# Kernel tuning notes

Measured on AMD Instinct MI355X. Metric: run time of the kernel, lower is better.

The kernel has to match this reference:

```python
import jax, jax.numpy as jnp
import numpy as np

N = 100000        # nodes
E = 3200000       # edges (avg degree 32)
D_IN, D_H, D_OUT = 128, 128, 64
EPS = 1e-5        # BatchNorm eps


def setup_inputs() -> dict:
    key = jax.random.key(0)
    ks = jax.random.split(key, 12)
    s = 0.1
    return {
        "x": jax.random.normal(ks[0], (N, D_IN), jnp.float32),
        "edge_index": jax.random.randint(ks[1], (2, E), 0, N, jnp.int32),
        "W1": jax.random.normal(ks[2], (D_IN, D_H), jnp.float32) * s,
        "b1": jnp.zeros((D_H,), jnp.float32),
        "W2": jax.random.normal(ks[3], (D_H, D_H), jnp.float32) * s,
        "b2": jnp.zeros((D_H,), jnp.float32),
        "W3": jax.random.normal(ks[4], (D_H, D_OUT), jnp.float32) * s,
        "b3": jnp.zeros((D_OUT,), jnp.float32),
        "g1": jnp.ones((D_H,), jnp.float32),
        "be1": jnp.zeros((D_H,), jnp.float32),
        "g2": jnp.ones((D_H,), jnp.float32),
        "be2": jnp.zeros((D_H,), jnp.float32),
    }


def reference(x, edge_index, W1, b1, W2, b2, W3, b3, g1, be1, g2, be2):
    # GCNConv normalization: add self-loops, symmetric deg^-1/2 A deg^-1/2
    loop = jnp.arange(N, dtype=edge_index.dtype)
    src = jnp.concatenate([edge_index[0], loop])   # [E+N]
    dst = jnp.concatenate([edge_index[1], loop])   # [E+N]
    deg = jax.ops.segment_sum(jnp.ones(src.shape, x.dtype), dst, num_segments=N)
    dinv = jnp.where(deg > 0, jax.lax.rsqrt(deg), 0.0)
    norm = (dinv[src] * dinv[dst])[:, None]        # [E+N, 1]

    def conv(h, W, b):
        h = h @ W                                   # dense transform [N, d]
        msg = h[src] * norm                         # gather + scale [E+N, d]
        return jax.ops.segment_sum(msg, dst, num_segments=N) + b

    def bn(h, g, be):  # BatchNorm1d over nodes (batch stats, eval-style dropout)
        m = h.mean(axis=0)
        v = h.var(axis=0)
        return (h - m) * jax.lax.rsqrt(v + EPS) * g + be

    h = jax.nn.relu(bn(conv(x, W1, b1), g1, be1))
    h = jax.nn.relu(bn(conv(h, W2, b2), g2, be2))
    h = conv(h, W3, b3)
    return jax.nn.softmax(h, axis=1)
```

## Files before the change

### kernel.cpp

```cpp
#include <hip/hip_runtime.h>
#include <hip/hip_fp16.h>

constexpr int   NN   = 100000;
constexpr int   NE   = 3200000;
constexpr float BN_EPS = 1e-5f;

constexpr int MG_B  = (NN / 32 + 3) / 4;
constexpr int CNT_B = NE / 256;
constexpr int SC_B  = NN * 128 / 4 / 256;

typedef _Float16 half8 __attribute__((ext_vector_type(8)));
typedef float    floatx16 __attribute__((ext_vector_type(16)));

__global__ __launch_bounds__(256) void k_wprep_all(const float* __restrict__ W1,
                                                   const float* __restrict__ W2,
                                                   const float* __restrict__ W3,
                                                   _Float16* __restrict__ Wt1,
                                                   _Float16* __restrict__ Wt2,
                                                   _Float16* __restrict__ Wt3) {
  int idx = blockIdx.x * 256 + threadIdx.x;
  if (idx < 16384) {
    int k = idx >> 7, n = idx & 127;
    Wt1[n * 128 + k] = (_Float16)W1[idx];
  } else if (idx < 32768) {
    int j = idx - 16384, k = j >> 7, n = j & 127;
    Wt2[n * 128 + k] = (_Float16)W2[j];
  } else if (idx < 40960) {
    int j = idx - 32768, k = j >> 6, n = j & 63;
    Wt3[n * 128 + k] = (_Float16)W3[j];
  }
}

__global__ __launch_bounds__(256) void k_f1(const int* __restrict__ dst,
                                            int* __restrict__ deg,
                                            int* __restrict__ slot,
                                            const float* __restrict__ x,
                                            const _Float16* __restrict__ Wt1,
                                            _Float16* __restrict__ C) {
  if (blockIdx.x < MG_B) {
    int wid  = (blockIdx.x * 256 + threadIdx.x) >> 6;
    int lane = threadIdx.x & 63;
    if (wid >= NN / 32) return;
    const int m = lane & 31;
    const int q = lane >> 5;
    const int row0 = wid * 32;
    const float* Arow = x + (size_t)(row0 + m) * 128 + q * 8;

    floatx16 acc[4] = {};
#pragma unroll
    for (int s = 0; s < 8; ++s) {
      float4 a0 = *(const float4*)(Arow + 16 * s);
      float4 a1 = *(const float4*)(Arow + 16 * s + 4);
      half8 af;
      af[0] = (_Float16)a0.x; af[1] = (_Float16)a0.y;
      af[2] = (_Float16)a0.z; af[3] = (_Float16)a0.w;
      af[4] = (_Float16)a1.x; af[5] = (_Float16)a1.y;
      af[6] = (_Float16)a1.z; af[7] = (_Float16)a1.w;
#pragma unroll
      for (int ct = 0; ct < 4; ++ct) {
        half8 bf = *(const half8*)(Wt1 + (size_t)(ct * 32 + m) * 128 + q * 8 + 16 * s);
        acc[ct] = __builtin_amdgcn_mfma_f32_32x32x16_f16(af, bf, acc[ct], 0, 0, 0);
      }
    }
#pragma unroll
    for (int ct = 0; ct < 4; ++ct)
#pragma unroll
      for (int r = 0; r < 16; ++r) {
        int row = (r & 3) + 8 * (r >> 2) + 4 * q;
        C[(size_t)(row0 + row) * 128 + ct * 32 + m] = (_Float16)acc[ct][r];
      }
  } else {
    int e = (blockIdx.x - MG_B) * 256 + threadIdx.x;
    if (e < NE) slot[e] = atomicAdd(&deg[dst[e]], 1);
  }
}

__global__ __launch_bounds__(256) void k_scan_a(const int* __restrict__ deg,
                                                float* __restrict__ dinv,
                                                int* __restrict__ rowptr,
                                                int* __restrict__ bsum) {
  __shared__ int sd[256];
  int t = threadIdx.x;
  int i = blockIdx.x * 256 + t;
  int v = (i < NN) ? deg[i] : 0;
  if (i < NN) dinv[i] = rsqrtf((float)(v + 1));
  sd[t] = v;
  __syncthreads();
  for (int off = 1; off < 256; off <<= 1) {
    int x = (t >= off) ? sd[t - off] : 0;
    __syncthreads();
    sd[t] += x;
    __syncthreads();
  }
  if (i < NN) rowptr[i] = sd[t] - v;
  if (t == 255) bsum[blockIdx.x] = sd[255];
}

__global__ __launch_bounds__(512) void k_scan_b(int* __restrict__ bsum, int nb) {
  __shared__ int sd[512];
  int t = threadIdx.x;
  int v = (t < nb) ? bsum[t] : 0;
  sd[t] = v;
  __syncthreads();
  for (int off = 1; off < 512; off <<= 1) {
    int x = (t >= off) ? sd[t - off] : 0;
    __syncthreads();
    sd[t] += x;
    __syncthreads();
  }
  if (t < nb) bsum[t] = sd[t] - v;
}

__global__ __launch_bounds__(256) void k_scan_c(int* __restrict__ rowptr,
                                                const int* __restrict__ bsum) {
  int i = blockIdx.x * 256 + threadIdx.x;
  if (i < NN) rowptr[i] += bsum[blockIdx.x];
  if (i == 0) rowptr[NN] = NE;
}

__global__ __launch_bounds__(256) void k_f2(const int* __restrict__ ei,
                                            const int* __restrict__ rowptr,
                                            const int* __restrict__ slot,
                                            int* __restrict__ csrc,
                                            const float* __restrict__ dinv,
                                            uint2* __restrict__ Hf) {
  if (blockIdx.x < SC_B) {
    int i = blockIdx.x * 256 + threadIdx.x;
    int row = i >> 5;
    float dv = dinv[row];
    uint2 v = Hf[i];
    __half2 h0 = *(__half2*)&v.x;
    __half2 h1 = *(__half2*)&v.y;
    float2 f0 = __half22float2(h0);
    float2 f1 = __half22float2(h1);
    h0 = __floats2half2_rn(f0.x * dv, f0.y * dv);
    h1 = __floats2half2_rn(f1.x * dv, f1.y * dv);
    v.x = *(unsigned*)&h0;
    v.y = *(unsigned*)&h1;
    Hf[i] = v;
  } else {
    int e = (blockIdx.x - SC_B) * 256 + threadIdx.x;
    if (e >= NE) return;
    int s = ei[e];
    int d = ei[NE + e];
    csrc[rowptr[d] + slot[e]] = s;
  }
}

template <int BN_>
__global__ __launch_bounds__(256) void k_mgemm(const _Float16* __restrict__ A,
                                               const _Float16* __restrict__ Wt,
                                               const float* __restrict__ scale,
                                               const float* __restrict__ shift,
                                               const float* __restrict__ dinv,
                                               _Float16* __restrict__ C) {
  constexpr int NCT = BN_ / 32;
  int wid  = (blockIdx.x * 256 + threadIdx.x) >> 6;
  int lane = threadIdx.x & 63;
  if (wid >= NN / 32) return;
  const int m = lane & 31;
  const int q = lane >> 5;
  const int row0 = wid * 32;

  const _Float16* Arow = A + (size_t)(row0 + m) * 128 + q * 8;

  floatx16 acc[NCT] = {};

#pragma unroll
  for (int s = 0; s < 8; ++s) {
    half8 raw = *(const half8*)(Arow + 16 * s);
    int k0 = 16 * s + q * 8;
    half8 af;
#pragma unroll
    for (int j = 0; j < 8; ++j) {
      float a = fmaxf(fmaf((float)raw[j], scale[k0 + j], shift[k0 + j]), 0.f);
      af[j] = (_Float16)a;
    }
#pragma unroll
    for (int ct = 0; ct < NCT; ++ct) {
      half8 bf = *(const half8*)(Wt + (size_t)(ct * 32 + m) * 128 + q * 8 + 16 * s);
      acc[ct] = __builtin_amdgcn_mfma_f32_32x32x16_f16(af, bf, acc[ct], 0, 0, 0);
    }
  }

#pragma unroll
  for (int ct = 0; ct < NCT; ++ct)
#pragma unroll
    for (int r = 0; r < 16; ++r) {
      int row = (r & 3) + 8 * (r >> 2) + 4 * q;
      float dv = dinv[row0 + row];
      C[(size_t)(row0 + row) * BN_ + ct * 32 + m] = (_Float16)(acc[ct][r] * dv);
    }
}

__global__ __launch_bounds__(256) void k_agg128(const __half* __restrict__ H,
                                                const float* __restrict__ dinv,
                                                const int* __restrict__ rowptr,
                                                const int* __restrict__ srcs,
                                                __half2* __restrict__ out) {
  int wid  = (blockIdx.x * 256 + threadIdx.x) >> 6;
  int lane = threadIdx.x & 63;
  if (wid >= NN) return;
  const __half2* Hp = (const __half2*)H;
  float2 acc = __half22float2(Hp[(size_t)wid * 64 + lane]);
  int beg = rowptr[wid], end = rowptr[wid + 1];
  int e = beg;
  int end8 = beg + ((end - beg) & ~7);
  for (; e < end8; e += 8) {
    __half2 v0 = Hp[(size_t)srcs[e+0] * 64 + lane];
    __half2 v1 = Hp[(size_t)srcs[e+1] * 64 + lane];
    __half2 v2 = Hp[(size_t)srcs[e+2] * 64 + lane];
    __half2 v3 = Hp[(size_t)srcs[e+3] * 64 + lane];
    __half2 v4 = Hp[(size_t)srcs[e+4] * 64 + lane];
    __half2 v5 = Hp[(size_t)srcs[e+5] * 64 + lane];
    __half2 v6 = Hp[(size_t)srcs[e+6] * 64 + lane];
    __half2 v7 = Hp[(size_t)srcs[e+7] * 64 + lane];
    float2 f0 = __half22float2(v0), f1 = __half22float2(v1);
    float2 f2 = __half22float2(v2), f3 = __half22float2(v3);
    float2 f4 = __half22float2(v4), f5 = __half22float2(v5);
    float2 f6 = __half22float2(v6), f7 = __half22float2(v7);
    acc.x += (f0.x + f1.x) + (f2.x + f3.x) + (f4.x + f5.x) + (f6.x + f7.x);
    acc.y += (f0.y + f1.y) + (f2.y + f3.y) + (f4.y + f5.y) + (f6.y + f7.y);
  }
  for (; e < end; ++e) {
    float2 f = __half22float2(Hp[(size_t)srcs[e] * 64 + lane]);
    acc.x += f.x; acc.y += f.y;
  }
  float di = dinv[wid];
  out[(size_t)wid * 64 + lane] = __floats2half2_rn(acc.x * di, acc.y * di);
}

__global__ __launch_bounds__(256) void k_agg64_softmax(const __half* __restrict__ H,
                                                       const float* __restrict__ dinv,
                                                       const int* __restrict__ rowptr,
                                                       const int* __restrict__ srcs,
                                                       const float* __restrict__ b3,
                                                       float* __restrict__ out) {
  int wid  = (blockIdx.x * 256 + threadIdx.x) >> 6;
  int lane = threadIdx.x & 63;
  if (wid >= NN) return;
  float acc = __half2float(H[(size_t)wid * 64 + lane]);
  int beg = rowptr[wid], end = rowptr[wid + 1];
  int e = beg;
  int end8 = beg + ((end - beg) & ~7);
  for (; e < end8; e += 8) {
    float v0 = __half2float(H[(size_t)srcs[e+0] * 64 + lane]);
    float v1 = __half2float(H[(size_t)srcs[e+1] * 64 + lane]);
    float v2 = __half2float(H[(size_t)srcs[e+2] * 64 + lane]);
    float v3 = __half2float(H[(size_t)srcs[e+3] * 64 + lane]);
    float v4 = __half2float(H[(size_t)srcs[e+4] * 64 + lane]);
    float v5 = __half2float(H[(size_t)srcs[e+5] * 64 + lane]);
    float v6 = __half2float(H[(size_t)srcs[e+6] * 64 + lane]);
    float v7 = __half2float(H[(size_t)srcs[e+7] * 64 + lane]);
    acc += (v0 + v1) + (v2 + v3) + (v4 + v5) + (v6 + v7);
  }
  for (; e < end; ++e)
    acc += __half2float(H[(size_t)srcs[e] * 64 + lane]);
  acc = acc * dinv[wid] + b3[lane];

  float m = acc;
#pragma unroll
  for (int off = 32; off > 0; off >>= 1) m = fmaxf(m, __shfl_xor(m, off));
  float ev = __expf(acc - m);
  float s = ev;
#pragma unroll
  for (int off = 32; off > 0; off >>= 1) s += __shfl_xor(s, off);
  out[(size_t)wid * 64 + lane] = ev / s;
}

__global__ __launch_bounds__(256) void k_stats(const __half2* __restrict__ H2,
                                               float* __restrict__ S1,
                                               float* __restrict__ S2) {
  int t = threadIdx.x;
  int p = t & 63;
  int r = t >> 6;
  float2 s1 = {0.f, 0.f}, s2 = {0.f, 0.f};
  for (int row = blockIdx.x * 4 + r; row < NN; row += gridDim.x * 4) {
    float2 v = __half22float2(H2[(size_t)row * 64 + p]);
    s1.x += v.x; s1.y += v.y;
    s2.x += v.x * v.x; s2.y += v.y * v.y;
  }
  __shared__ float2 l1[256], l2[256];
  l1[t] = s1; l2[t] = s2;
  __syncthreads();
  if (t < 128) {
    l1[t].x += l1[t+128].x; l1[t].y += l1[t+128].y;
    l2[t].x += l2[t+128].x; l2[t].y += l2[t+128].y;
  }
  __syncthreads();
  if (t < 64) {
    float2 a1 = l1[t], b1 = l1[t+64];
    float2 a2 = l2[t], b2 = l2[t+64];
    atomicAdd(&S1[2*p+0], a1.x + b1.x);
    atomicAdd(&S1[2*p+1], a1.y + b1.y);
    atomicAdd(&S2[2*p+0], a2.x + b2.x);
    atomicAdd(&S2[2*p+1], a2.y + b2.y);
  }
}

__global__ void k_finalize(const float* __restrict__ S1, const float* __restrict__ S2,
                           const float* __restrict__ g,  const float* __restrict__ be,
                           float* __restrict__ scale,    float* __restrict__ shift) {
  int t = threadIdx.x;
  float mean = S1[t] * (1.0f / NN);
  float var  = S2[t] * (1.0f / NN) - mean * mean;
  float is   = rsqrtf(var + BN_EPS);
  float sc   = g[t] * is;
  scale[t] = sc;
  shift[t] = be[t] - mean * sc;
}

extern "C" void kernel_launch(void* const* d_in, const int* in_sizes, int n_in,
                              void* d_out, int out_size, void* d_ws, size_t ws_size,
                              hipStream_t stream) {
  (void)in_sizes; (void)n_in; (void)out_size; (void)ws_size;
  const float* x   = (const float*)d_in[0];
  const int*   ei  = (const int*)d_in[1];
  const float* W1  = (const float*)d_in[2];
  const float* W2  = (const float*)d_in[4];
  const float* W3  = (const float*)d_in[6];
  const float* b3  = (const float*)d_in[7];
  const float* g1  = (const float*)d_in[8];
  const float* be1 = (const float*)d_in[9];
  const float* g2  = (const float*)d_in[10];
  const float* be2 = (const float*)d_in[11];
  float* out = (float*)d_out;

  char* ws = (char*)d_ws;
  size_t off = 0;
  auto take = [&](size_t bytes) -> char* {
    char* p = ws + off;
    off = (off + bytes + 255) & ~(size_t)255;
    return p;
  };
  int*   deg    = (int*)  take((size_t)NN * 4);
  float* S1a    = (float*)take(128 * 4);
  float* S2a    = (float*)take(128 * 4);
  float* S1b    = (float*)take(128 * 4);
  float* S2b    = (float*)take(128 * 4);
  size_t zero_bytes = off;
  float* scale1 = (float*)take(128 * 4);
  float* shift1 = (float*)take(128 * 4);
  float* scale2 = (float*)take(128 * 4);
  float* shift2 = (float*)take(128 * 4);
  float* dinv   = (float*)take((size_t)NN * 4);
  int*   rowptr = (int*)  take((size_t)(NN + 1) * 4);
  int*   bsum   = (int*)  take(1024 * 4);
  int*   slot   = (int*)  take((size_t)NE * 4);
  int*   csrc   = (int*)  take((size_t)NE * 4);
  _Float16* Wt1 = (_Float16*)take((size_t)128 * 128 * 2);
  _Float16* Wt2 = (_Float16*)take((size_t)128 * 128 * 2);
  _Float16* Wt3 = (_Float16*)take((size_t)64 * 128 * 2);
  _Float16* Hf  = (_Float16*)take((size_t)NN * 128 * 2);
  _Float16* hB  = (_Float16*)take((size_t)NN * 128 * 2);

  (void)hipMemsetAsync(d_ws, 0, zero_bytes, stream);

  const int nbN  = (NN + 255) / 256;
  const int mgB  = MG_B;
  const int aggB = (NN + 3) / 4;

  k_wprep_all<<<160, 256, 0, stream>>>(W1, W2, W3, Wt1, Wt2, Wt3);

  k_f1<<<MG_B + CNT_B, 256, 0, stream>>>(ei + NE, deg, slot, x, Wt1, Hf);

  k_scan_a<<<nbN, 256, 0, stream>>>(deg, dinv, rowptr, bsum);
  k_scan_b<<<1, 512, 0, stream>>>(bsum, nbN);
  k_scan_c<<<nbN, 256, 0, stream>>>(rowptr, bsum);

  k_f2<<<SC_B + CNT_B, 256, 0, stream>>>(ei, rowptr, slot, csrc, dinv, (uint2*)Hf);

  k_agg128<<<aggB, 256, 0, stream>>>((const __half*)Hf, dinv, rowptr, csrc, (__half2*)hB);
  k_stats<<<1024, 256, 0, stream>>>((const __half2*)hB, S1a, S2a);
  k_finalize<<<1, 128, 0, stream>>>(S1a, S2a, g1, be1, scale1, shift1);

  k_mgemm<128><<<mgB, 256, 0, stream>>>(hB, Wt2, scale1, shift1, dinv, Hf);
  k_agg128<<<aggB, 256, 0, stream>>>((const __half*)Hf, dinv, rowptr, csrc, (__half2*)hB);
  k_stats<<<1024, 256, 0, stream>>>((const __half2*)hB, S1b, S2b);
  k_finalize<<<1, 128, 0, stream>>>(S1b, S2b, g2, be2, scale2, shift2);

  k_mgemm<64><<<mgB, 256, 0, stream>>>(hB, Wt3, scale2, shift2, dinv, Hf);
  k_agg64_softmax<<<aggB, 256, 0, stream>>>((const __half*)Hf, dinv, rowptr, csrc, b3, out);
}
```

Baseline: 837.8 us.

## Pack two nodes per wavefront in aggregation and merge scan into one kernel

The aggregation kernels now handle two destination nodes per 64-lane wavefront. Each half-wave gathers wider vectors (4 halves per lane for the 128-wide case, 2 per lane for the 64-wide softmax case), with predicated loads so both halves loop to the larger degree. This raises bytes per load instruction and the number of in-flight gathers per wave, at the cost of idle lanes when the two nodes' degrees differ. Separately, the three-kernel prefix scan is replaced by a single 1024-thread block that scans serial chunks, removing two launches but running the scan on one CU.

```diff
diff --git a/kernel.cpp b/kernel.cpp
--- a/kernel.cpp
+++ b/kernel.cpp
@@ -75,47 +75,31 @@
   }
 }
 
-__global__ __launch_bounds__(256) void k_scan_a(const int* __restrict__ deg,
-                                                float* __restrict__ dinv,
-                                                int* __restrict__ rowptr,
-                                                int* __restrict__ bsum) {
-  __shared__ int sd[256];
+__global__ __launch_bounds__(1024) void k_scan(const int* __restrict__ deg,
+                                               float* __restrict__ dinv,
+                                               int* __restrict__ rowptr) {
+  __shared__ int sd[1024];
   int t = threadIdx.x;
-  int i = blockIdx.x * 256 + t;
-  int v = (i < NN) ? deg[i] : 0;
-  if (i < NN) dinv[i] = rsqrtf((float)(v + 1));
-  sd[t] = v;
+  constexpr int CH = (NN + 1023) / 1024;
+  int b = t * CH, e = min(b + CH, NN);
+  int sum = 0;
+  for (int i = b; i < e; ++i) sum += deg[i];
+  sd[t] = sum;
   __syncthreads();
-  for (int off = 1; off < 256; off <<= 1) {
+  for (int off = 1; off < 1024; off <<= 1) {
     int x = (t >= off) ? sd[t - off] : 0;
     __syncthreads();
     sd[t] += x;
     __syncthreads();
   }
-  if (i < NN) rowptr[i] = sd[t] - v;
-  if (t == 255) bsum[blockIdx.x] = sd[255];
-}
-
-__global__ __launch_bounds__(512) void k_scan_b(int* __restrict__ bsum, int nb) {
-  __shared__ int sd[512];
-  int t = threadIdx.x;
-  int v = (t < nb) ? bsum[t] : 0;
-  sd[t] = v;
-  __syncthreads();
-  for (int off = 1; off < 512; off <<= 1) {
-    int x = (t >= off) ? sd[t - off] : 0;
-    __syncthreads();
-    sd[t] += x;
-    __syncthreads();
-  }
-  if (t < nb) bsum[t] = sd[t] - v;
-}
-
-__global__ __launch_bounds__(256) void k_scan_c(int* __restrict__ rowptr,
-                                                const int* __restrict__ bsum) {
-  int i = blockIdx.x * 256 + threadIdx.x;
-  if (i < NN) rowptr[i] += bsum[blockIdx.x];
-  if (i == 0) rowptr[NN] = NE;
+  int run = sd[t] - sum;
+  for (int i = b; i < e; ++i) {
+    int d = deg[i];
+    rowptr[i] = run;
+    run += d;
+    dinv[i] = rsqrtf((float)(d + 1));
+  }
+  if (t == 1023) rowptr[NN] = NE;
 }
 
 __global__ __launch_bounds__(256) void k_f2(const int* __restrict__ ei,
@@ -193,79 +177,96 @@
     }
 }
 
-__global__ __launch_bounds__(256) void k_agg128(const __half* __restrict__ H,
-                                                const float* __restrict__ dinv,
-                                                const int* __restrict__ rowptr,
-                                                const int* __restrict__ srcs,
-                                                __half2* __restrict__ out) {
-  int wid  = (blockIdx.x * 256 + threadIdx.x) >> 6;
+__global__ __launch_bounds__(256) void k_agg128p(const __half* __restrict__ H,
+                                                 const float* __restrict__ dinv,
+                                                 const int* __restrict__ rowptr,
+                                                 const int* __restrict__ srcs,
+                                                 uint2* __restrict__ out) {
+  int pw   = (blockIdx.x * 256 + threadIdx.x) >> 6;
   int lane = threadIdx.x & 63;
-  if (wid >= NN) return;
+  if (pw >= NN / 2) return;
+  const int half = lane >> 5;
+  const int node = pw * 2 + half;
+  const int c4   = lane & 31;
+  const uint2* Hp = (const uint2*)H;
+
+  uint2 sv = Hp[(size_t)node * 32 + c4];
+  __half2 s0 = *(__half2*)&sv.x, s1 = *(__half2*)&sv.y;
+  float2 a01 = __half22float2(s0);
+  float2 a23 = __half22float2(s1);
+
+  int beg = rowptr[node];
+  int cnt = rowptr[node + 1] - beg;
+  int cmax = max(__shfl(cnt, 0), __shfl(cnt, 32));
+
+  for (int i = 0; i < cmax; i += 4) {
+#pragma unroll
+    for (int j = 0; j < 4; ++j) {
+      bool p = (i + j) < cnt;
+      int pos = min(beg + (p ? i + j : 0), NE - 1);
+      int s = srcs[pos];
+      uint2 v = Hp[(size_t)s * 32 + c4];
+      __half2 h0 = *(__half2*)&v.x, h1 = *(__half2*)&v.y;
+      float2 f01 = __half22float2(h0);
+      float2 f23 = __half22float2(h1);
+      if (p) {
+        a01.x += f01.x; a01.y += f01.y;
+        a23.x += f23.x; a23.y += f23.y;
+      }
+    }
+  }
+  float di = dinv[node];
+  __half2 o0 = __floats2half2_rn(a01.x * di, a01.y * di);
+  __half2 o1 = __floats2half2_rn(a23.x * di, a23.y * di);
+  uint2 ov;
+  ov.x = *(unsigned*)&o0;
+  ov.y = *(unsigned*)&o1;
+  out[(size_t)node * 32 + c4] = ov;
+}
+
+__global__ __launch_bounds__(256) void k_agg64p_softmax(const __half* __restrict__ H,
+                                                        const float* __restrict__ dinv,
+                                                        const int* __restrict__ rowptr,
+                                                        const int* __restrict__ srcs,
+                                                        const float* __restrict__ b3,
+                                                        float* __restrict__ out) {
+  int pw   = (blockIdx.x * 256 + threadIdx.x) >> 6;
+  int lane = threadIdx.x & 63;
+  if (pw >= NN / 2) return;
+  const int half = lane >> 5;
+  const int node = pw * 2 + half;
+  const int c2   = lane & 31;
   const __half2* Hp = (const __half2*)H;
-  float2 acc = __half22float2(Hp[(size_t)wid * 64 + lane]);
-  int beg = rowptr[wid], end = rowptr[wid + 1];
-  int e = beg;
-  int end8 = beg + ((end - beg) & ~7);
-  for (; e < end8; e += 8) {
-    __half2 v0 = Hp[(size_t)srcs[e+0] * 64 + lane];
-    __half2 v1 = Hp[(size_t)srcs[e+1] * 64 + lane];
-    __half2 v2 = Hp[(size_t)srcs[e+2] * 64 + lane];
-    __half2 v3 = Hp[(size_t)srcs[e+3] * 64 + lane];
-    __half2 v4 = Hp[(size_t)srcs[e+4] * 64 + lane];
-    __half2 v5 = Hp[(size_t)srcs[e+5] * 64 + lane];
-    __half2 v6 = Hp[(size_t)srcs[e+6] * 64 + lane];
-    __half2 v7 = Hp[(size_t)srcs[e+7] * 64 + lane];
-    float2 f0 = __half22float2(v0), f1 = __half22float2(v1);
-    float2 f2 = __half22float2(v2), f3 = __half22float2(v3);
-    float2 f4 = __half22float2(v4), f5 = __half22float2(v5);
-    float2 f6 = __half22float2(v6), f7 = __half22float2(v7);
-    acc.x += (f0.x + f1.x) + (f2.x + f3.x) + (f4.x + f5.x) + (f6.x + f7.x);
-    acc.y += (f0.y + f1.y) + (f2.y + f3.y) + (f4.y + f5.y) + (f6.y + f7.y);
-  }
-  for (; e < end; ++e) {
-    float2 f = __half22float2(Hp[(size_t)srcs[e] * 64 + lane]);
-    acc.x += f.x; acc.y += f.y;
-  }
-  float di = dinv[wid];
-  out[(size_t)wid * 64 + lane] = __floats2half2_rn(acc.x * di, acc.y * di);
-}
-
-__global__ __launch_bounds__(256) void k_agg64_softmax(const __half* __restrict__ H,
-                                                       const float* __restrict__ dinv,
-                                                       const int* __restrict__ rowptr,
-                                                       const int* __restrict__ srcs,
-                                                       const float* __restrict__ b3,
-                                                       float* __restrict__ out) {
-  int wid  = (blockIdx.x * 256 + threadIdx.x) >> 6;
-  int lane = threadIdx.x & 63;
-  if (wid >= NN) return;
-  float acc = __half2float(H[(size_t)wid * 64 + lane]);
-  int beg = rowptr[wid], end = rowptr[wid + 1];
-  int e = beg;
-  int end8 = beg + ((end - beg) & ~7);
-  for (; e < end8; e += 8) {
-    float v0 = __half2float(H[(size_t)srcs[e+0] * 64 + lane]);
-    float v1 = __half2float(H[(size_t)srcs[e+1] * 64 + lane]);
-    float v2 = __half2float(H[(size_t)srcs[e+2] * 64 + lane]);
-    float v3 = __half2float(H[(size_t)srcs[e+3] * 64 + lane]);
-    float v4 = __half2float(H[(size_t)srcs[e+4] * 64 + lane]);
-    float v5 = __half2float(H[(size_t)srcs[e+5] * 64 + lane]);
-    float v6 = __half2float(H[(size_t)srcs[e+6] * 64 + lane]);
-    float v7 = __half2float(H[(size_t)srcs[e+7] * 64 + lane]);
-    acc += (v0 + v1) + (v2 + v3) + (v4 + v5) + (v6 + v7);
-  }
-  for (; e < end; ++e)
-    acc += __half2float(H[(size_t)srcs[e] * 64 + lane]);
-  acc = acc * dinv[wid] + b3[lane];
-
-  float m = acc;
-#pragma unroll
-  for (int off = 32; off > 0; off >>= 1) m = fmaxf(m, __shfl_xor(m, off));
-  float ev = __expf(acc - m);
-  float s = ev;
-#pragma unroll
-  for (int off = 32; off > 0; off >>= 1) s += __shfl_xor(s, off);
-  out[(size_t)wid * 64 + lane] = ev / s;
+
+  float2 acc = __half22float2(Hp[(size_t)node * 32 + c2]);
+
+  int beg = rowptr[node];
+  int cnt = rowptr[node + 1] - beg;
+  int cmax = max(__shfl(cnt, 0), __shfl(cnt, 32));
+
+  for (int i = 0; i < cmax; i += 4) {
+#pragma unroll
+    for (int j = 0; j < 4; ++j) {
+      bool p = (i + j) < cnt;
+      int pos = min(beg + (p ? i + j : 0), NE - 1);
+      int s = srcs[pos];
+      float2 f = __half22float2(Hp[(size_t)s * 32 + c2]);
+      if (p) { acc.x += f.x; acc.y += f.y; }
+    }
+  }
+  float di = dinv[node];
+  float l0 = acc.x * di + b3[2 * c2];
+  float l1 = acc.y * di + b3[2 * c2 + 1];
+
+  float m = fmaxf(l0, l1);
+#pragma unroll
+  for (int off = 16; off > 0; off >>= 1) m = fmaxf(m, __shfl_xor(m, off));
+  float e0 = __expf(l0 - m), e1 = __expf(l1 - m);
+  float s = e0 + e1;
+#pragma unroll
+  for (int off = 16; off > 0; off >>= 1) s += __shfl_xor(s, off);
+  float inv = 1.0f / s;
+  ((float2*)out)[(size_t)node * 32 + c2] = make_float2(e0 * inv, e1 * inv);
 }
 
 __global__ __launch_bounds__(256) void k_stats(const __half2* __restrict__ H2,
@@ -345,7 +346,6 @@
   float* shift2 = (float*)take(128 * 4);
   float* dinv   = (float*)take((size_t)NN * 4);
   int*   rowptr = (int*)  take((size_t)(NN + 1) * 4);
-  int*   bsum   = (int*)  take(1024 * 4);
   int*   slot   = (int*)  take((size_t)NE * 4);
   int*   csrc   = (int*)  take((size_t)NE * 4);
   _Float16* Wt1 = (_Float16*)take((size_t)128 * 128 * 2);
@@ -356,29 +356,26 @@
 
   (void)hipMemsetAsync(d_ws, 0, zero_bytes, stream);
 
-  const int nbN  = (NN + 255) / 256;
   const int mgB  = MG_B;
-  const int aggB = (NN + 3) / 4;
+  const int aggB = (NN / 2 + 3) / 4;
 
   k_wprep_all<<<160, 256, 0, stream>>>(W1, W2, W3, Wt1, Wt2, Wt3);
 
   k_f1<<<MG_B + CNT_B, 256, 0, stream>>>(ei + NE, deg, slot, x, Wt1, Hf);
 
-  k_scan_a<<<nbN, 256, 0, stream>>>(deg, dinv, rowptr, bsum);
-  k_scan_b<<<1, 512, 0, stream>>>(bsum, nbN);
-  k_scan_c<<<nbN, 256, 0, stream>>>(rowptr, bsum);
+  k_scan<<<1, 1024, 0, stream>>>(deg, dinv, rowptr);
 
   k_f2<<<SC_B + CNT_B, 256, 0, stream>>>(ei, rowptr, slot, csrc, dinv, (uint2*)Hf);
 
-  k_agg128<<<aggB, 256, 0, stream>>>((const __half*)Hf, dinv, rowptr, csrc, (__half2*)hB);
+  k_agg128p<<<aggB, 256, 0, stream>>>((const __half*)Hf, dinv, rowptr, csrc, (uint2*)hB);
   k_stats<<<1024, 256, 0, stream>>>((const __half2*)hB, S1a, S2a);
   k_finalize<<<1, 128, 0, stream>>>(S1a, S2a, g1, be1, scale1, shift1);
 
   k_mgemm<128><<<mgB, 256, 0, stream>>>(hB, Wt2, scale1, shift1, dinv, Hf);
-  k_agg128<<<aggB, 256, 0, stream>>>((const __half*)Hf, dinv, rowptr, csrc, (__half2*)hB);
+  k_agg128p<<<aggB, 256, 0, stream>>>((const __half*)Hf, dinv, rowptr, csrc, (uint2*)hB);
   k_stats<<<1024, 256, 0, stream>>>((const __half2*)hB, S1b, S2b);
   k_finalize<<<1, 128, 0, stream>>>(S1b, S2b, g2, be2, scale2, shift2);
 
   k_mgemm<64><<<mgB, 256, 0, stream>>>(hB, Wt3, scale2, shift2, dinv, Hf);
-  k_agg64_softmax<<<aggB, 256, 0, stream>>>((const __half*)Hf, dinv, rowptr, csrc, b3, out);
-}
+  k_agg64p_softmax<<<aggB, 256, 0, stream>>>((const __half*)Hf, dinv, rowptr, csrc, b3, out);
+}
```

Result: slower. 1.184 ms (+41.4%).

## Fuse BatchNorm statistics into aggregation and finalize into GEMM prologue

Applied to the files above, without the earlier changes.

Merges the neighbor-aggregation kernel with the BatchNorm sum and sum-of-squares reduction. It uses a grid-stride persistent layout with 2048 blocks and accumulates statistics in registers before one set of atomics per block. The separate stats and finalize kernels are removed, and each GEMM block now computes the scale and shift into shared memory from the raw sums. This saves a full re-read of the hidden activations and four launches per forward pass. In exchange, the aggregation grid becomes fixed-size grid-stride, which may change load balance and latency hiding, and every GEMM block redundantly recomputes the finalize.

```diff
diff --git a/kernel.cpp b/kernel.cpp
--- a/kernel.cpp
+++ b/kernel.cpp
@@ -147,14 +147,86 @@
   }
 }
 
+__global__ __launch_bounds__(256) void k_aggstats(const __half* __restrict__ H,
+                                                  const float* __restrict__ dinv,
+                                                  const int* __restrict__ rowptr,
+                                                  const int* __restrict__ srcs,
+                                                  __half2* __restrict__ out,
+                                                  float* __restrict__ S1,
+                                                  float* __restrict__ S2) {
+  int lane = threadIdx.x & 63;
+  int wv   = threadIdx.x >> 6;
+  const __half2* Hp = (const __half2*)H;
+  float2 s1 = {0.f, 0.f}, s2 = {0.f, 0.f};
+
+  for (int node = blockIdx.x * 4 + wv; node < NN; node += gridDim.x * 4) {
+    float2 acc = __half22float2(Hp[(size_t)node * 64 + lane]);
+    int beg = rowptr[node], end = rowptr[node + 1];
+    int e = beg;
+    int end8 = beg + ((end - beg) & ~7);
+    for (; e < end8; e += 8) {
+      __half2 v0 = Hp[(size_t)srcs[e+0] * 64 + lane];
+      __half2 v1 = Hp[(size_t)srcs[e+1] * 64 + lane];
+      __half2 v2 = Hp[(size_t)srcs[e+2] * 64 + lane];
+      __half2 v3 = Hp[(size_t)srcs[e+3] * 64 + lane];
+      __half2 v4 = Hp[(size_t)srcs[e+4] * 64 + lane];
+      __half2 v5 = Hp[(size_t)srcs[e+5] * 64 + lane];
+      __half2 v6 = Hp[(size_t)srcs[e+6] * 64 + lane];
+      __half2 v7 = Hp[(size_t)srcs[e+7] * 64 + lane];
+      float2 f0 = __half22float2(v0), f1 = __half22float2(v1);
+      float2 f2 = __half22float2(v2), f3 = __half22float2(v3);
+      float2 f4 = __half22float2(v4), f5 = __half22float2(v5);
+      float2 f6 = __half22float2(v6), f7 = __half22float2(v7);
+      acc.x += (f0.x + f1.x) + (f2.x + f3.x) + (f4.x + f5.x) + (f6.x + f7.x);
+      acc.y += (f0.y + f1.y) + (f2.y + f3.y) + (f4.y + f5.y) + (f6.y + f7.y);
+    }
+    for (; e < end; ++e) {
+      float2 f = __half22float2(Hp[(size_t)srcs[e] * 64 + lane]);
+      acc.x += f.x; acc.y += f.y;
+    }
+    float di = dinv[node];
+    float hx = acc.x * di, hy = acc.y * di;
+    out[(size_t)node * 64 + lane] = __floats2half2_rn(hx, hy);
+    s1.x += hx; s1.y += hy;
+    s2.x += hx * hx; s2.y += hy * hy;
+  }
+
+  __shared__ float2 l1[256], l2[256];
+  l1[threadIdx.x] = s1; l2[threadIdx.x] = s2;
+  __syncthreads();
+  int t = threadIdx.x;
+  if (t < 64) {
+    float2 a1 = l1[t], b1 = l1[t+64], c1 = l1[t+128], d1 = l1[t+192];
+    float2 a2 = l2[t], b2 = l2[t+64], c2 = l2[t+128], d2 = l2[t+192];
+    atomicAdd(&S1[2*t+0], (a1.x + b1.x) + (c1.x + d1.x));
+    atomicAdd(&S1[2*t+1], (a1.y + b1.y) + (c1.y + d1.y));
+    atomicAdd(&S2[2*t+0], (a2.x + b2.x) + (c2.x + d2.x));
+    atomicAdd(&S2[2*t+1], (a2.y + b2.y) + (c2.y + d2.y));
+  }
+}
+
 template <int BN_>
 __global__ __launch_bounds__(256) void k_mgemm(const _Float16* __restrict__ A,
                                                const _Float16* __restrict__ Wt,
-                                               const float* __restrict__ scale,
-                                               const float* __restrict__ shift,
+                                               const float* __restrict__ S1,
+                                               const float* __restrict__ S2,
+                                               const float* __restrict__ g,
+                                               const float* __restrict__ be,
                                                const float* __restrict__ dinv,
                                                _Float16* __restrict__ C) {
   constexpr int NCT = BN_ / 32;
+  __shared__ float sc[128], sh[128];
+  int t = threadIdx.x;
+  if (t < 128) {
+    float mean = S1[t] * (1.0f / NN);
+    float var  = S2[t] * (1.0f / NN) - mean * mean;
+    float is   = rsqrtf(var + BN_EPS);
+    float s    = g[t] * is;
+    sc[t] = s;
+    sh[t] = be[t] - mean * s;
+  }
+  __syncthreads();
+
   int wid  = (blockIdx.x * 256 + threadIdx.x) >> 6;
   int lane = threadIdx.x & 63;
   if (wid >= NN / 32) return;
@@ -173,7 +245,7 @@
     half8 af;
 #pragma unroll
     for (int j = 0; j < 8; ++j) {
-      float a = fmaxf(fmaf((float)raw[j], scale[k0 + j], shift[k0 + j]), 0.f);
+      float a = fmaxf(fmaf((float)raw[j], sc[k0 + j], sh[k0 + j]), 0.f);
       af[j] = (_Float16)a;
     }
 #pragma unroll
@@ -191,43 +263,6 @@
       float dv = dinv[row0 + row];
       C[(size_t)(row0 + row) * BN_ + ct * 32 + m] = (_Float16)(acc[ct][r] * dv);
     }
-}
-
-__global__ __launch_bounds__(256) void k_agg128(const __half* __restrict__ H,
-                                                const float* __restrict__ dinv,
-                                                const int* __restrict__ rowptr,
-                                                const int* __restrict__ srcs,
-                                                __half2* __restrict__ out) {
-  int wid  = (blockIdx.x * 256 + threadIdx.x) >> 6;
-  int lane = threadIdx.x & 63;
-  if (wid >= NN) return;
-  const __half2* Hp = (const __half2*)H;
-  float2 acc = __half22float2(Hp[(size_t)wid * 64 + lane]);
-  int beg = rowptr[wid], end = rowptr[wid + 1];
-  int e = beg;
-  int end8 = beg + ((end - beg) & ~7);
-  for (; e < end8; e += 8) {
-    __half2 v0 = Hp[(size_t)srcs[e+0] * 64 + lane];
-    __half2 v1 = Hp[(size_t)srcs[e+1] * 64 + lane];
-    __half2 v2 = Hp[(size_t)srcs[e+2] * 64 + lane];
-    __half2 v3 = Hp[(size_t)srcs[e+3] * 64 + lane];
-    __half2 v4 = Hp[(size_t)srcs[e+4] * 64 + lane];
-    __half2 v5 = Hp[(size_t)srcs[e+5] * 64 + lane];
-    __half2 v6 = Hp[(size_t)srcs[e+6] * 64 + lane];
-    __half2 v7 = Hp[(size_t)srcs[e+7] * 64 + lane];
-    float2 f0 = __half22float2(v0), f1 = __half22float2(v1);
-    float2 f2 = __half22float2(v2), f3 = __half22float2(v3);
-    float2 f4 = __half22float2(v4), f5 = __half22float2(v5);
-    float2 f6 = __half22float2(v6), f7 = __half22float2(v7);
-    acc.x += (f0.x + f1.x) + (f2.x + f3.x) + (f4.x + f5.x) + (f6.x + f7.x);
-    acc.y += (f0.y + f1.y) + (f2.y + f3.y) + (f4.y + f5.y) + (f6.y + f7.y);
-  }
-  for (; e < end; ++e) {
-    float2 f = __half22float2(Hp[(size_t)srcs[e] * 64 + lane]);
-    acc.x += f.x; acc.y += f.y;
-  }
-  float di = dinv[wid];
-  out[(size_t)wid * 64 + lane] = __floats2half2_rn(acc.x * di, acc.y * di);
 }
 
 __global__ __launch_bounds__(256) void k_agg64_softmax(const __half* __restrict__ H,
@@ -268,48 +303,6 @@
   out[(size_t)wid * 64 + lane] = ev / s;
 }
 
-__global__ __launch_bounds__(256) void k_stats(const __half2* __restrict__ H2,
-                                               float* __restrict__ S1,
-                                               float* __restrict__ S2) {
-  int t = threadIdx.x;
-  int p = t & 63;
-  int r = t >> 6;
-  float2 s1 = {0.f, 0.f}, s2 = {0.f, 0.f};
-  for (int row = blockIdx.x * 4 + r; row < NN; row += gridDim.x * 4) {
-    float2 v = __half22float2(H2[(size_t)row * 64 + p]);
-    s1.x += v.x; s1.y += v.y;
-    s2.x += v.x * v.x; s2.y += v.y * v.y;
-  }
-  __shared__ float2 l1[256], l2[256];
-  l1[t] = s1; l2[t] = s2;
-  __syncthreads();
-  if (t < 128) {
-    l1[t].x += l1[t+128].x; l1[t].y += l1[t+128].y;
-    l2[t].x += l2[t+128].x; l2[t].y += l2[t+128].y;
-  }
-  __syncthreads();
-  if (t < 64) {
-    float2 a1 = l1[t], b1 = l1[t+64];
-    float2 a2 = l2[t], b2 = l2[t+64];
-    atomicAdd(&S1[2*p+0], a1.x + b1.x);
-    atomicAdd(&S1[2*p+1], a1.y + b1.y);
-    atomicAdd(&S2[2*p+0], a2.x + b2.x);
-    atomicAdd(&S2[2*p+1], a2.y + b2.y);
-  }
-}
-
-__global__ void k_finalize(const float* __restrict__ S1, const float* __restrict__ S2,
-                           const float* __restrict__ g,  const float* __restrict__ be,
-                           float* __restrict__ scale,    float* __restrict__ shift) {
-  int t = threadIdx.x;
-  float mean = S1[t] * (1.0f / NN);
-  float var  = S2[t] * (1.0f / NN) - mean * mean;
-  float is   = rsqrtf(var + BN_EPS);
-  float sc   = g[t] * is;
-  scale[t] = sc;
-  shift[t] = be[t] - mean * sc;
-}
-
 extern "C" void kernel_launch(void* const* d_in, const int* in_sizes, int n_in,
                               void* d_out, int out_size, void* d_ws, size_t ws_size,
                               hipStream_t stream) {
@@ -339,10 +332,6 @@
   float* S1b    = (float*)take(128 * 4);
   float* S2b    = (float*)take(128 * 4);
   size_t zero_bytes = off;
-  float* scale1 = (float*)take(128 * 4);
-  float* shift1 = (float*)take(128 * 4);
-  float* scale2 = (float*)take(128 * 4);
-  float* shift2 = (float*)take(128 * 4);
   float* dinv   = (float*)take((size_t)NN * 4);
   int*   rowptr = (int*)  take((size_t)(NN + 1) * 4);
   int*   bsum   = (int*)  take(1024 * 4);
@@ -357,7 +346,6 @@
   (void)hipMemsetAsync(d_ws, 0, zero_bytes, stream);
 
   const int nbN  = (NN + 255) / 256;
-  const int mgB  = MG_B;
   const int aggB = (NN + 3) / 4;
 
   k_wprep_all<<<160, 256, 0, stream>>>(W1, W2, W3, Wt1, Wt2, Wt3);
@@ -370,15 +358,13 @@
 
   k_f2<<<SC_B + CNT_B, 256, 0, stream>>>(ei, rowptr, slot, csrc, dinv, (uint2*)Hf);
 
-  k_agg128<<<aggB, 256, 0, stream>>>((const __half*)Hf, dinv, rowptr, csrc, (__half2*)hB);
-  k_stats<<<1024, 256, 0, stream>>>((const __half2*)hB, S1a, S2a);
-  k_finalize<<<1, 128, 0, stream>>>(S1a, S2a, g1, be1, scale1, shift1);
-
-  k_mgemm<128><<<mgB, 256, 0, stream>>>(hB, Wt2, scale1, shift1, dinv, Hf);
-  k_agg128<<<aggB, 256, 0, stream>>>((const __half*)Hf, dinv, rowptr, csrc, (__half2*)hB);
-  k_stats<<<1024, 256, 0, stream>>>((const __half2*)hB, S1b, S2b);
-  k_finalize<<<1, 128, 0, stream>>>(S1b, S2b, g2, be2, scale2, shift2);
-
-  k_mgemm<64><<<mgB, 256, 0, stream>>>(hB, Wt3, scale2, shift2, dinv, Hf);
+  k_aggstats<<<2048, 256, 0, stream>>>((const __half*)Hf, dinv, rowptr, csrc,
+                                       (__half2*)hB, S1a, S2a);
+
+  k_mgemm<128><<<MG_B, 256, 0, stream>>>(hB, Wt2, S1a, S2a, g1, be1, dinv, Hf);
+  k_aggstats<<<2048, 256, 0, stream>>>((const __half*)Hf, dinv, rowptr, csrc,
+                                       (__half2*)hB, S1b, S2b);
+
+  k_mgemm<64><<<MG_B, 256, 0, stream>>>(hB, Wt3, S1b, S2b, g2, be2, dinv, Hf);
   k_agg64_softmax<<<aggB, 256, 0, stream>>>((const __half*)Hf, dinv, rowptr, csrc, b3, out);
 }
```

Result: slower. 885.3 us (+5.7%).
